# Optimization experiments

Measured on AMD Instinct MI355X. Metric: run time of the kernel, lower is better.

Reference implementation:

```python
import jax, jax.numpy as jnp
import numpy as np

H = 1024      # hidden_size
I = 2048      # intermediate_size
E = 8         # num_local_experts
TOP_K = 2     # num_experts_per_tok
B, S = 2, 2048


def setup_inputs() -> dict:
    key = jax.random.key(0)
    ks = jax.random.split(key, 9)
    sc = 0.02
    return {
        "hidden_states": jax.random.normal(ks[0], (B, S, H), dtype=jnp.float32),
        "router_w": jax.random.normal(ks[1], (H, E), dtype=jnp.float32) * sc,
        "gate_w": jax.random.normal(ks[2], (E, H, I), dtype=jnp.float32) * sc,
        "up_w": jax.random.normal(ks[3], (E, H, I), dtype=jnp.float32) * sc,
        "down_w": jax.random.normal(ks[4], (E, I, H), dtype=jnp.float32) * sc,
        "shared_gate_w": jax.random.normal(ks[5], (H, I), dtype=jnp.float32) * sc,
        "shared_up_w": jax.random.normal(ks[6], (H, I), dtype=jnp.float32) * sc,
        "shared_down_w": jax.random.normal(ks[7], (I, H), dtype=jnp.float32) * sc,
    }


def reference(hidden_states, router_w, gate_w, up_w, down_w,
              shared_gate_w, shared_up_w, shared_down_w):
    b, s, h = hidden_states.shape
    T = b * s
    x = hidden_states.reshape(T, h)

    # Router
    router_logits = x @ router_w                                   # [T, E]
    router_probs = jax.nn.softmax(router_logits.astype(jnp.float32), axis=-1).astype(x.dtype)
    topk_w, topk_i = jax.lax.top_k(router_probs, TOP_K)            # [T, K]
    topk_w = topk_w / jnp.sum(topk_w, axis=-1, keepdims=True)

    # Combine weights: combine[t, e] = sum of normalized top-k weight routed to expert e
    rows = jnp.arange(T)[:, None]
    combine = jnp.zeros((T, E), dtype=x.dtype).at[rows, topk_i].add(topk_w)  # [T, E]

    # Dense per-expert SwiGLU (combine weight is 0 for non-selected tokens, so
    # this matches the original gather-MLP-scatter math exactly)
    gate = jax.nn.silu(jnp.einsum('th,ehi->tei', x, gate_w))       # [T, E, I]
    up = jnp.einsum('th,ehi->tei', x, up_w)                        # [T, E, I]
    expert_out = jnp.einsum('tei,eih->teh', gate * up, down_w)     # [T, E, H]
    routed = jnp.einsum('te,teh->th', combine, expert_out)         # [T, H]

    # Shared expert (num_shared_experts = 1, mean over 1 is identity)
    shared = (jax.nn.silu(x @ shared_gate_w) * (x @ shared_up_w)) @ shared_down_w
    routed = routed + shared

    # Load-balance aux loss
    dispatch = jax.nn.one_hot(topk_i, E, dtype=jnp.float32).sum(axis=1) / float(TOP_K)  # [T, E]
    tokens_per_expert = dispatch.mean(axis=0)
    prob_per_expert = router_probs.astype(jnp.float32).mean(axis=0)
    aux_loss = E * jnp.sum(tokens_per_expert * prob_per_expert)

    # Router z-loss
    z_loss = jnp.mean(jax.nn.logsumexp(router_logits.astype(jnp.float32), axis=-1) ** 2)

    return (routed.reshape(b, s, h), aux_loss, z_loss,
            router_logits.reshape(b, s, E))
```

## Files before the change

kernel.cpp:

```cpp
#include <hip/hip_runtime.h>
#include <hip/hip_bf16.h>
#include <stdint.h>
#include <stddef.h>

typedef __bf16 bf16;
typedef __bf16 bf16x8 __attribute__((ext_vector_type(8)));
typedef __bf16 bf16x4 __attribute__((ext_vector_type(4)));
typedef float f32x4 __attribute__((ext_vector_type(4)));

#define HID 1024
#define IDIM 2048
#define NE 8
#define NTOK 4096
#define NSLOT 13312
#define SH_BASE 9216
#define MAX_TILES 104

#define WS_META    0
#define WS_PERM    4096
#define WS_TOKE    57344
#define WS_TOKW    90112
#define WS_SLOTOF  122880
#define WS_XBF     155648
#define WS_GATET   8544256
#define WS_UPT     42098688
#define WS_DOWNT   75653120
#define WS_SGT     109207552
#define WS_SUT     113401856
#define WS_SDT     117596160
#define WS_ACT     121790464
#define WS_DOUT    WS_GATET

#define M_CNT 0
#define M_CUR 8
#define M_PSUM 16
#define M_ZSUM 24
#define M_AOFF 32
#define M_NTILE 48
#define M_TE 64
#define M_TB 320

#define OUT_AUX 4194304
#define OUT_Z   4194305
#define OUT_LG  4194306

__device__ __forceinline__ int imin(int a, int b) { return a < b ? a : b; }

typedef const __attribute__((address_space(1))) uint32_t* as1_u32p;
typedef __attribute__((address_space(3))) uint32_t* as3_u32p;

__device__ __forceinline__ void gload16(const void* g, void* l) {
    __builtin_amdgcn_global_load_lds((as1_u32p)g, (as3_u32p)l, 16, 0, 0);
}

__global__ void zero_kernel(uint32_t* meta) {
    if (threadIdx.x < 32) meta[threadIdx.x] = 0;
}

__global__ __launch_bounds__(1024) void router_kernel(
    const float* __restrict__ x, const float* __restrict__ rw,
    float* __restrict__ out, uint32_t* meta, int* tok_e, float* tok_w,
    bf16* __restrict__ xbf)
{
    __shared__ float s_psum[NE];
    __shared__ float s_zsum;
    __shared__ uint32_t s_cnt[NE];
    int tid = threadIdx.x;
    if (tid < NE) { s_psum[tid] = 0.f; s_cnt[tid] = 0u; }
    if (tid == NE) s_zsum = 0.f;
    __syncthreads();

    int lane = tid & 63, wv = tid >> 6;
    int t = blockIdx.x * 16 + wv;
    float acc[NE];
#pragma unroll
    for (int e = 0; e < NE; e++) acc[e] = 0.f;
#pragma unroll
    for (int it = 0; it < 4; it++) {
        int h0 = (lane + it * 64) * 4;
        f32x4 xv = *(const f32x4*)&x[(size_t)t * HID + h0];
        bf16x4 xb;
#pragma unroll
        for (int j = 0; j < 4; j++) xb[j] = (bf16)xv[j];
        *(bf16x4*)&xbf[(size_t)t * HID + h0] = xb;
#pragma unroll
        for (int j = 0; j < 4; j++) {
            float xf = xv[j];
            const float* wrow = rw + (size_t)(h0 + j) * NE;
            f32x4 w0 = *(const f32x4*)wrow;
            f32x4 w1 = *(const f32x4*)(wrow + 4);
#pragma unroll
            for (int e = 0; e < 4; e++) { acc[e] += xf * w0[e]; acc[e + 4] += xf * w1[e]; }
        }
    }
#pragma unroll
    for (int off = 32; off >= 1; off >>= 1)
#pragma unroll
        for (int e = 0; e < NE; e++) acc[e] += __shfl_xor(acc[e], off);

    if (lane == 0) {
        float mx = acc[0];
        for (int e = 1; e < NE; e++) mx = fmaxf(mx, acc[e]);
        float p[NE], s = 0.f;
        for (int e = 0; e < NE; e++) { p[e] = __expf(acc[e] - mx); s += p[e]; }
        float lse = mx + __logf(s);
        atomicAdd(&s_zsum, lse * lse);
        float inv = 1.f / s;
        for (int e = 0; e < NE; e++) {
            p[e] *= inv;
            atomicAdd(&s_psum[e], p[e]);
            out[(size_t)OUT_LG + (size_t)t * NE + e] = acc[e];
        }
        int e0 = 0;
        for (int e = 1; e < NE; e++) if (p[e] > p[e0]) e0 = e;
        int e1 = (e0 == 0) ? 1 : 0;
        for (int e = 0; e < NE; e++) if (e != e0 && p[e] > p[e1]) e1 = e;
        float wn = 1.f / (p[e0] + p[e1]);
        tok_e[2 * t] = e0; tok_e[2 * t + 1] = e1;
        tok_w[2 * t] = p[e0] * wn; tok_w[2 * t + 1] = p[e1] * wn;
        atomicAdd(&s_cnt[e0], 1u);
        atomicAdd(&s_cnt[e1], 1u);
    }
    __syncthreads();
    if (tid < NE) {
        atomicAdd((float*)&meta[M_PSUM + tid], s_psum[tid]);
        atomicAdd(&meta[M_CNT + tid], s_cnt[tid]);
    }
    if (tid == NE) atomicAdd((float*)&meta[M_ZSUM], s_zsum);
}

__global__ void offsets_kernel(uint32_t* meta, float* out) {
    __shared__ uint32_t s_aoff[NE + 1];
    int lane = threadIdx.x;
    if (lane == 0) {
        uint32_t off = 0;
        for (int e = 0; e < NE; e++) {
            meta[M_AOFF + e] = off; s_aoff[e] = off;
            off += ((meta[M_CNT + e] + 127) >> 7) << 7;
        }
        meta[M_AOFF + NE] = off; s_aoff[NE] = off;
        float aux = 0.f;
        for (int e = 0; e < NE; e++) {
            float tpe = (float)meta[M_CNT + e] / (2.f * NTOK);
            float ppe = ((float*)meta)[M_PSUM + e] / (float)NTOK;
            aux += tpe * ppe;
        }
        out[OUT_AUX] = aux * NE;
        out[OUT_Z] = ((float*)meta)[M_ZSUM] / (float)NTOK;
    }
    __syncthreads();
    uint32_t nrt = s_aoff[NE] >> 7;
    uint32_t ntile = nrt + NTOK / 128;
    if (lane == 0) meta[M_NTILE] = ntile;
    for (uint32_t idx = lane; idx < ntile && idx < MAX_TILES; idx += 64) {
        if (idx < nrt) {
            uint32_t base = idx << 7, e = 0;
            for (int j = 1; j < NE; j++) if (base >= s_aoff[j]) e = j;
            meta[M_TE + idx] = e;
            meta[M_TB + idx] = base;
        } else {
            meta[M_TE + idx] = NE;
            meta[M_TB + idx] = SH_BASE + ((idx - nrt) << 7);
        }
    }
}

__global__ void fill_kernel(uint32_t* perm) {
    int g = blockIdx.x * 256 + threadIdx.x;
    if (g < NSLOT) perm[g] = (g < SH_BASE) ? 0u : (uint32_t)(g - SH_BASE);
}

__global__ void dispatch_kernel(uint32_t* meta, const int* tok_e,
                                uint32_t* perm, uint32_t* slot_of) {
    int t = blockIdx.x * 256 + threadIdx.x;
    int lane = threadIdx.x & 63;
    for (int k = 0; k < 2; k++) {
        int e = tok_e[2 * t + k] & 7;
#pragma unroll
        for (int ee = 0; ee < NE; ee++) {
            bool mine = (e == ee);
            unsigned long long mask = __ballot(mine);
            if (mask == 0ull) continue;
            int leader = __ffsll((unsigned long long)mask) - 1;
            uint32_t wbase = 0;
            if (lane == leader)
                wbase = atomicAdd(&meta[M_CUR + ee], (uint32_t)__popcll(mask));
            wbase = __shfl(wbase, leader);
            if (mine) {
                uint32_t myrank = (uint32_t)__popcll(mask & ((1ull << lane) - 1ull));
                uint32_t slot = meta[M_AOFF + ee] + wbase + myrank;
                if (slot >= NSLOT) slot = 0;
                perm[slot] = (uint32_t)t;
                slot_of[2 * t + k] = slot;
            }
        }
    }
}

__device__ __forceinline__ size_t f_off(int n, int k, int KB32) {
    return ((size_t)((n >> 5) * KB32 + (k >> 5)) * 2 + ((n >> 4) & 1)) * 512
         + (size_t)((((k >> 3) & 3) * 16 + (n & 15)) * 8);
}

__global__ __launch_bounds__(256) void transpose_kernel(
    const float* gw, const float* uw, const float* dw,
    const float* sg, const float* su, const float* sd, char* ws)
{
    int mat = blockIdx.x >> 9, tile = blockIdx.x & 511;
    const float* src; bf16* dst; int R, C;
    const size_t MSZ = (size_t)HID * IDIM;
    if (mat < 8)       { src = gw + mat * MSZ;        dst = (bf16*)(ws + WS_GATET) + mat * MSZ; R = HID;  C = IDIM; }
    else if (mat < 16) { src = uw + (mat - 8) * MSZ;  dst = (bf16*)(ws + WS_UPT) + (mat - 8) * MSZ; R = HID; C = IDIM; }
    else if (mat < 24) { src = dw + (mat - 16) * MSZ; dst = (bf16*)(ws + WS_DOWNT) + (mat - 16) * MSZ; R = IDIM; C = HID; }
    else if (mat == 24){ src = sg; dst = (bf16*)(ws + WS_SGT); R = HID; C = IDIM; }
    else if (mat == 25){ src = su; dst = (bf16*)(ws + WS_SUT); R = HID; C = IDIM; }
    else               { src = sd; dst = (bf16*)(ws + WS_SDT); R = IDIM; C = HID; }
    int KB32 = R >> 5;
    int tpr = C >> 6;
    int r0 = (tile / tpr) * 64, c0 = (tile % tpr) * 64;
    __shared__ bf16 tl[64][65];
    int tid = threadIdx.x;
#pragma unroll
    for (int it = 0; it < 4; it++) {
        int idx = tid + it * 256;
        int r = idx >> 4, c4 = (idx & 15) * 4;
        f32x4 v = *(const f32x4*)&src[(size_t)(r0 + r) * C + c0 + c4];
#pragma unroll
        for (int j = 0; j < 4; j++) tl[c4 + j][r] = (bf16)v[j];
    }
    __syncthreads();
#pragma unroll
    for (int it = 0; it < 2; it++) {
        int idx = tid + it * 256;
        int rr = idx >> 3, c8 = (idx & 7) * 8;
        int n = c0 + rr, k = r0 + c8;
        bf16x8 o;
#pragma unroll
        for (int j = 0; j < 8; j++) o[j] = tl[rr][c8 + j];
        *(bf16x8*)&dst[f_off(n, k, KB32)] = o;
    }
}

__global__ __launch_bounds__(256, 2) void stage1_kernel(char* __restrict__ ws)
{
    uint32_t* meta = (uint32_t*)(ws + WS_META);
    int mtile = blockIdx.y;
    int ntile = imin((int)meta[M_NTILE], MAX_TILES);
    if (mtile >= ntile) return;
    int e = imin((int)meta[M_TE + mtile], NE);
    int slot0 = imin((int)meta[M_TB + mtile], NSLOT - 128);
    if (slot0 < 0) slot0 = 0;
    const bf16* BgF = (e < NE) ? (const bf16*)(ws + WS_GATET) + (size_t)e * HID * IDIM
                               : (const bf16*)(ws + WS_SGT);
    const bf16* BuF = (e < NE) ? (const bf16*)(ws + WS_UPT) + (size_t)e * HID * IDIM
                               : (const bf16*)(ws + WS_SUT);
    const uint32_t* perm = (const uint32_t*)(ws + WS_PERM);
    const bf16* xbf = (const bf16*)(ws + WS_XBF);
    bf16* act = (bf16*)(ws + WS_ACT);

    __shared__ bf16 As[8192];
    __shared__ bf16 Bgs[8192];
    __shared__ bf16 Bus[8192];

    int tid = threadIdx.x, lane = tid & 63, wv = tid >> 6;
    int q = lane >> 4, m = lane & 15;

    int tok0 = (int)(perm[slot0 + wv * 16 + m] & (NTOK - 1));
    int tok1 = (int)(perm[slot0 + (wv + 4) * 16 + m] & (NTOK - 1));
    const bf16* gA0 = xbf + (size_t)tok0 * HID + q * 8;
    const bf16* gA1 = xbf + (size_t)tok1 * HID + q * 8;
    int N32 = blockIdx.x * 4 + wv;
    const bf16* gBg = BgF + (size_t)N32 * 32768 + lane * 8;
    const bf16* gBu = BuF + (size_t)N32 * 32768 + lane * 8;

    f32x4 zero4 = {0.f, 0.f, 0.f, 0.f};
    f32x4 accg[8][2], accu[8][2];
#pragma unroll
    for (int a = 0; a < 8; a++)
#pragma unroll
        for (int b = 0; b < 2; b++) { accg[a][b] = zero4; accu[a][b] = zero4; }

    for (int k0 = 0; k0 < HID; k0 += 64) {
        int kc = k0 >> 5;
        gload16(gA0 + k0,      &As[(wv * 2 + 0) * 512]);
        gload16(gA0 + k0 + 32, &As[(wv * 2 + 1) * 512]);
        gload16(gA1 + k0,      &As[((wv + 4) * 2 + 0) * 512]);
        gload16(gA1 + k0 + 32, &As[((wv + 4) * 2 + 1) * 512]);
#pragma unroll
        for (int nt = 0; nt < 2; nt++)
#pragma unroll
            for (int kk = 0; kk < 2; kk++) {
                size_t so = (size_t)(kc + kk) * 1024 + nt * 512;
                gload16(gBg + so, &Bgs[((wv * 2 + nt) * 2 + kk) * 512]);
                gload16(gBu + so, &Bus[((wv * 2 + nt) * 2 + kk) * 512]);
            }
        __syncthreads();
#pragma unroll
        for (int kk = 0; kk < 2; kk++) {
            bf16x8 af[8];
#pragma unroll
            for (int mc = 0; mc < 8; mc++)
                af[mc] = *(bf16x8*)&As[((mc * 2 + kk) * 64 + lane) * 8];
#pragma unroll
            for (int nt = 0; nt < 2; nt++) {
                bf16x8 bg = *(bf16x8*)&Bgs[(((wv * 2 + nt) * 2 + kk) * 64 + lane) * 8];
                bf16x8 bu = *(bf16x8*)&Bus[(((wv * 2 + nt) * 2 + kk) * 64 + lane) * 8];
#pragma unroll
                for (int mc = 0; mc < 8; mc++) {
                    accg[mc][nt] = __builtin_amdgcn_mfma_f32_16x16x32_bf16(af[mc], bg, accg[mc][nt], 0, 0, 0);
                    accu[mc][nt] = __builtin_amdgcn_mfma_f32_16x16x32_bf16(af[mc], bu, accu[mc][nt], 0, 0, 0);
                }
            }
        }
        __syncthreads();
    }
    int tile = slot0 >> 7;
    int kcell = blockIdx.x * 4 + wv;
    size_t tbase = (size_t)tile * 262144;
#pragma unroll
    for (int mc = 0; mc < 8; mc++)
#pragma unroll
        for (int nt = 0; nt < 2; nt++) {
            int kc2 = nt * 2 + (m >> 3);
            size_t base = tbase + (size_t)(kcell * 8 + mc) * 512
                        + (size_t)(kc2 * 16) * 8 + (m & 7);
#pragma unroll
            for (int r = 0; r < 4; r++) {
                float g = accg[mc][nt][r], u = accu[mc][nt][r];
                float v = g / (1.f + __expf(-g)) * u;
                act[base + (size_t)(q * 4 + r) * 8] = (bf16)v;
            }
        }
}

__global__ __launch_bounds__(256, 3) void stage2_kernel(char* __restrict__ ws)
{
    uint32_t* meta = (uint32_t*)(ws + WS_META);
    int mtile = blockIdx.y;
    int ntile = imin((int)meta[M_NTILE], MAX_TILES);
    if (mtile >= ntile) return;
    int e = imin((int)meta[M_TE + mtile], NE);
    int slot0 = imin((int)meta[M_TB + mtile], NSLOT - 128);
    if (slot0 < 0) slot0 = 0;
    int n0 = blockIdx.x * 128;
    const bf16* BF = (e < NE) ? (const bf16*)(ws + WS_DOWNT) + (size_t)e * HID * IDIM
                              : (const bf16*)(ws + WS_SDT);
    const bf16* actF = (const bf16*)(ws + WS_ACT);
    bf16* dout = (bf16*)(ws + WS_DOUT);

    __shared__ bf16 As[8192];
    __shared__ bf16 Bs[8192];

    int tid = threadIdx.x, lane = tid & 63, wv = tid >> 6;
    int q = lane >> 4, m = lane & 15;

    int tile = slot0 >> 7;
    size_t tbase = (size_t)tile * 262144;
    const bf16* gA = actF + tbase + lane * 8;
    int N32 = blockIdx.x * 4 + wv;
    const bf16* gB = BF + (size_t)N32 * 65536 + lane * 8;

    f32x4 zero4 = {0.f, 0.f, 0.f, 0.f};
    f32x4 acc[8][2];
#pragma unroll
    for (int a = 0; a < 8; a++)
#pragma unroll
        for (int b = 0; b < 2; b++) acc[a][b] = zero4;

    for (int k0 = 0; k0 < IDIM; k0 += 64) {
        int kc = k0 >> 5;
#pragma unroll
        for (int kk = 0; kk < 2; kk++) {
            gload16(gA + (size_t)((kc + kk) * 8 + wv) * 512,     &As[(wv * 2 + kk) * 512]);
            gload16(gA + (size_t)((kc + kk) * 8 + wv + 4) * 512, &As[((wv + 4) * 2 + kk) * 512]);
        }
#pragma unroll
        for (int nt = 0; nt < 2; nt++)
#pragma unroll
            for (int kk = 0; kk < 2; kk++)
                gload16(gB + (size_t)(kc + kk) * 1024 + nt * 512,
                        &Bs[((wv * 2 + nt) * 2 + kk) * 512]);
        __syncthreads();
#pragma unroll
        for (int kk = 0; kk < 2; kk++) {
            bf16x8 af[8];
#pragma unroll
            for (int mc = 0; mc < 8; mc++)
                af[mc] = *(bf16x8*)&As[((mc * 2 + kk) * 64 + lane) * 8];
#pragma unroll
            for (int nt = 0; nt < 2; nt++) {
                bf16x8 bfr = *(bf16x8*)&Bs[(((wv * 2 + nt) * 2 + kk) * 64 + lane) * 8];
#pragma unroll
                for (int mc = 0; mc < 8; mc++)
                    acc[mc][nt] = __builtin_amdgcn_mfma_f32_16x16x32_bf16(af[mc], bfr, acc[mc][nt], 0, 0, 0);
            }
        }
        __syncthreads();
    }
#pragma unroll
    for (int mc = 0; mc < 8; mc++)
#pragma unroll
        for (int nt = 0; nt < 2; nt++)
#pragma unroll
            for (int r = 0; r < 4; r++) {
                int slot = slot0 + mc * 16 + q * 4 + r;
                int col = n0 + wv * 32 + nt * 16 + m;
                dout[(size_t)slot * HID + col] = (bf16)acc[mc][nt][r];
            }
}

__global__ __launch_bounds__(256) void combine_kernel(char* __restrict__ ws, float* __restrict__ out)
{
    int g = blockIdx.x * 256 + threadIdx.x;
    int t = g >> 7;
    int hc = (g & 127) * 8;
    const uint32_t* slot_of = (const uint32_t*)(ws + WS_SLOTOF);
    const float* tok_w = (const float*)(ws + WS_TOKW);
    const bf16* dout = (const bf16*)(ws + WS_DOUT);
    uint32_t s0 = slot_of[2 * t], s1 = slot_of[2 * t + 1];
    if (s0 >= NSLOT) s0 = 0;
    if (s1 >= NSLOT) s1 = 0;
    float w0 = tok_w[2 * t], w1 = tok_w[2 * t + 1];
    bf16x8 a = *(const bf16x8*)&dout[(size_t)s0 * HID + hc];
    bf16x8 b = *(const bf16x8*)&dout[(size_t)s1 * HID + hc];
    bf16x8 c = *(const bf16x8*)&dout[(size_t)(SH_BASE + t) * HID + hc];
    f32x4 o0, o1;
#pragma unroll
    for (int j = 0; j < 4; j++)
        o0[j] = w0 * (float)a[j] + w1 * (float)b[j] + (float)c[j];
#pragma unroll
    for (int j = 0; j < 4; j++)
        o1[j] = w0 * (float)a[j + 4] + w1 * (float)b[j + 4] + (float)c[j + 4];
    *(f32x4*)&out[(size_t)t * HID + hc] = o0;
    *(f32x4*)&out[(size_t)t * HID + hc + 4] = o1;
}

extern "C" void kernel_launch(void* const* d_in, const int* in_sizes, int n_in,
                              void* d_out, int out_size, void* d_ws, size_t ws_size,
                              hipStream_t stream) {
    const float* x  = (const float*)d_in[0];
    const float* rw = (const float*)d_in[1];
    const float* gw = (const float*)d_in[2];
    const float* uw = (const float*)d_in[3];
    const float* dw = (const float*)d_in[4];
    const float* sg = (const float*)d_in[5];
    const float* su = (const float*)d_in[6];
    const float* sd = (const float*)d_in[7];
    float* out = (float*)d_out;
    char* ws = (char*)d_ws;
    uint32_t* meta = (uint32_t*)(ws + WS_META);
    uint32_t* perm = (uint32_t*)(ws + WS_PERM);
    int* tok_e = (int*)(ws + WS_TOKE);
    float* tok_w = (float*)(ws + WS_TOKW);
    uint32_t* slot_of = (uint32_t*)(ws + WS_SLOTOF);
    bf16* xbf = (bf16*)(ws + WS_XBF);

    hipLaunchKernelGGL(zero_kernel, dim3(1), dim3(64), 0, stream, meta);
    hipLaunchKernelGGL(router_kernel, dim3(NTOK / 16), dim3(1024), 0, stream,
                       x, rw, out, meta, tok_e, tok_w, xbf);
    hipLaunchKernelGGL(offsets_kernel, dim3(1), dim3(64), 0, stream, meta, out);
    hipLaunchKernelGGL(fill_kernel, dim3((NSLOT + 255) / 256), dim3(256), 0, stream, perm);
    hipLaunchKernelGGL(dispatch_kernel, dim3(NTOK / 256), dim3(256), 0, stream,
                       meta, tok_e, perm, slot_of);
    hipLaunchKernelGGL(transpose_kernel, dim3(27 * 512), dim3(256), 0, stream,
                       gw, uw, dw, sg, su, sd, ws);
    hipLaunchKernelGGL(stage1_kernel, dim3(IDIM / 128, MAX_TILES), dim3(256), 0, stream, ws);
    hipLaunchKernelGGL(stage2_kernel, dim3(HID / 128, MAX_TILES), dim3(256), 0, stream, ws);
    hipLaunchKernelGGL(combine_kernel, dim3(NTOK * HID / 8 / 256), dim3(256), 0, stream, ws, out);
}
```

Baseline: 509.1 us.

## Load MFMA operands directly from global memory, drop LDS staging in expert GEMMs

```diff
diff --git a/kernel.cpp b/kernel.cpp
--- a/kernel.cpp
+++ b/kernel.cpp
@@ -45,13 +45,6 @@
 #define OUT_LG  4194306
 
 __device__ __forceinline__ int imin(int a, int b) { return a < b ? a : b; }
-
-typedef const __attribute__((address_space(1))) uint32_t* as1_u32p;
-typedef __attribute__((address_space(3))) uint32_t* as3_u32p;
-
-__device__ __forceinline__ void gload16(const void* g, void* l) {
-    __builtin_amdgcn_global_load_lds((as1_u32p)g, (as3_u32p)l, 16, 0, 0);
-}
 
 __global__ void zero_kernel(uint32_t* meta) {
     if (threadIdx.x < 32) meta[threadIdx.x] = 0;
@@ -258,17 +251,15 @@
     const bf16* xbf = (const bf16*)(ws + WS_XBF);
     bf16* act = (bf16*)(ws + WS_ACT);
 
-    __shared__ bf16 As[8192];
-    __shared__ bf16 Bgs[8192];
-    __shared__ bf16 Bus[8192];
-
     int tid = threadIdx.x, lane = tid & 63, wv = tid >> 6;
     int q = lane >> 4, m = lane & 15;
 
-    int tok0 = (int)(perm[slot0 + wv * 16 + m] & (NTOK - 1));
-    int tok1 = (int)(perm[slot0 + (wv + 4) * 16 + m] & (NTOK - 1));
-    const bf16* gA0 = xbf + (size_t)tok0 * HID + q * 8;
-    const bf16* gA1 = xbf + (size_t)tok1 * HID + q * 8;
+    const bf16* ga[8];
+#pragma unroll
+    for (int mc = 0; mc < 8; mc++) {
+        int tok = (int)(perm[slot0 + mc * 16 + m] & (NTOK - 1));
+        ga[mc] = xbf + (size_t)tok * HID + q * 8;
+    }
     int N32 = blockIdx.x * 4 + wv;
     const bf16* gBg = BgF + (size_t)N32 * 32768 + lane * 8;
     const bf16* gBu = BuF + (size_t)N32 * 32768 + lane * 8;
@@ -280,39 +271,27 @@
 #pragma unroll
         for (int b = 0; b < 2; b++) { accg[a][b] = zero4; accu[a][b] = zero4; }
 
-    for (int k0 = 0; k0 < HID; k0 += 64) {
-        int kc = k0 >> 5;
-        gload16(gA0 + k0,      &As[(wv * 2 + 0) * 512]);
-        gload16(gA0 + k0 + 32, &As[(wv * 2 + 1) * 512]);
-        gload16(gA1 + k0,      &As[((wv + 4) * 2 + 0) * 512]);
-        gload16(gA1 + k0 + 32, &As[((wv + 4) * 2 + 1) * 512]);
-#pragma unroll
-        for (int nt = 0; nt < 2; nt++)
-#pragma unroll
-            for (int kk = 0; kk < 2; kk++) {
-                size_t so = (size_t)(kc + kk) * 1024 + nt * 512;
-                gload16(gBg + so, &Bgs[((wv * 2 + nt) * 2 + kk) * 512]);
-                gload16(gBu + so, &Bus[((wv * 2 + nt) * 2 + kk) * 512]);
+    for (int kc = 0; kc < 32; kc += 2) {
+#pragma unroll
+        for (int kk = 0; kk < 2; kk++) {
+            int k = (kc + kk) * 32;
+            bf16x8 af[8];
+#pragma unroll
+            for (int mc = 0; mc < 8; mc++)
+                af[mc] = *(const bf16x8*)(ga[mc] + k);
+            size_t bo = (size_t)(kc + kk) * 1024;
+            bf16x8 bg0 = *(const bf16x8*)(gBg + bo);
+            bf16x8 bg1 = *(const bf16x8*)(gBg + bo + 512);
+            bf16x8 bu0 = *(const bf16x8*)(gBu + bo);
+            bf16x8 bu1 = *(const bf16x8*)(gBu + bo + 512);
+#pragma unroll
+            for (int mc = 0; mc < 8; mc++) {
+                accg[mc][0] = __builtin_amdgcn_mfma_f32_16x16x32_bf16(af[mc], bg0, accg[mc][0], 0, 0, 0);
+                accg[mc][1] = __builtin_amdgcn_mfma_f32_16x16x32_bf16(af[mc], bg1, accg[mc][1], 0, 0, 0);
+                accu[mc][0] = __builtin_amdgcn_mfma_f32_16x16x32_bf16(af[mc], bu0, accu[mc][0], 0, 0, 0);
+                accu[mc][1] = __builtin_amdgcn_mfma_f32_16x16x32_bf16(af[mc], bu1, accu[mc][1], 0, 0, 0);
             }
-        __syncthreads();
-#pragma unroll
-        for (int kk = 0; kk < 2; kk++) {
-            bf16x8 af[8];
-#pragma unroll
-            for (int mc = 0; mc < 8; mc++)
-                af[mc] = *(bf16x8*)&As[((mc * 2 + kk) * 64 + lane) * 8];
-#pragma unroll
-            for (int nt = 0; nt < 2; nt++) {
-                bf16x8 bg = *(bf16x8*)&Bgs[(((wv * 2 + nt) * 2 + kk) * 64 + lane) * 8];
-                bf16x8 bu = *(bf16x8*)&Bus[(((wv * 2 + nt) * 2 + kk) * 64 + lane) * 8];
-#pragma unroll
-                for (int mc = 0; mc < 8; mc++) {
-                    accg[mc][nt] = __builtin_amdgcn_mfma_f32_16x16x32_bf16(af[mc], bg, accg[mc][nt], 0, 0, 0);
-                    accu[mc][nt] = __builtin_amdgcn_mfma_f32_16x16x32_bf16(af[mc], bu, accu[mc][nt], 0, 0, 0);
-                }
-            }
-        }
-        __syncthreads();
+        }
     }
     int tile = slot0 >> 7;
     int kcell = blockIdx.x * 4 + wv;
@@ -333,7 +312,7 @@
         }
 }
 
-__global__ __launch_bounds__(256, 3) void stage2_kernel(char* __restrict__ ws)
+__global__ __launch_bounds__(256, 2) void stage2_kernel(char* __restrict__ ws)
 {
     uint32_t* meta = (uint32_t*)(ws + WS_META);
     int mtile = blockIdx.y;
@@ -342,69 +321,58 @@
     int e = imin((int)meta[M_TE + mtile], NE);
     int slot0 = imin((int)meta[M_TB + mtile], NSLOT - 128);
     if (slot0 < 0) slot0 = 0;
-    int n0 = blockIdx.x * 128;
+    int n0 = blockIdx.x * 256;
     const bf16* BF = (e < NE) ? (const bf16*)(ws + WS_DOWNT) + (size_t)e * HID * IDIM
                               : (const bf16*)(ws + WS_SDT);
     const bf16* actF = (const bf16*)(ws + WS_ACT);
     bf16* dout = (bf16*)(ws + WS_DOUT);
 
-    __shared__ bf16 As[8192];
-    __shared__ bf16 Bs[8192];
-
     int tid = threadIdx.x, lane = tid & 63, wv = tid >> 6;
     int q = lane >> 4, m = lane & 15;
 
     int tile = slot0 >> 7;
-    size_t tbase = (size_t)tile * 262144;
-    const bf16* gA = actF + tbase + lane * 8;
-    int N32 = blockIdx.x * 4 + wv;
-    const bf16* gB = BF + (size_t)N32 * 65536 + lane * 8;
+    const bf16* gA = actF + (size_t)tile * 262144 + lane * 8;
+    int n32a = blockIdx.x * 8 + wv * 2;
+    const bf16* gB0 = BF + (size_t)n32a * 65536 + lane * 8;
+    const bf16* gB1 = BF + (size_t)(n32a + 1) * 65536 + lane * 8;
 
     f32x4 zero4 = {0.f, 0.f, 0.f, 0.f};
-    f32x4 acc[8][2];
+    f32x4 acc[8][4];
 #pragma unroll
     for (int a = 0; a < 8; a++)
 #pragma unroll
-        for (int b = 0; b < 2; b++) acc[a][b] = zero4;
-
-    for (int k0 = 0; k0 < IDIM; k0 += 64) {
-        int kc = k0 >> 5;
+        for (int b = 0; b < 4; b++) acc[a][b] = zero4;
+
+    for (int kc = 0; kc < 64; kc += 2) {
 #pragma unroll
         for (int kk = 0; kk < 2; kk++) {
-            gload16(gA + (size_t)((kc + kk) * 8 + wv) * 512,     &As[(wv * 2 + kk) * 512]);
-            gload16(gA + (size_t)((kc + kk) * 8 + wv + 4) * 512, &As[((wv + 4) * 2 + kk) * 512]);
-        }
-#pragma unroll
-        for (int nt = 0; nt < 2; nt++)
-#pragma unroll
-            for (int kk = 0; kk < 2; kk++)
-                gload16(gB + (size_t)(kc + kk) * 1024 + nt * 512,
-                        &Bs[((wv * 2 + nt) * 2 + kk) * 512]);
-        __syncthreads();
-#pragma unroll
-        for (int kk = 0; kk < 2; kk++) {
+            int kcc = kc + kk;
             bf16x8 af[8];
 #pragma unroll
             for (int mc = 0; mc < 8; mc++)
-                af[mc] = *(bf16x8*)&As[((mc * 2 + kk) * 64 + lane) * 8];
-#pragma unroll
-            for (int nt = 0; nt < 2; nt++) {
-                bf16x8 bfr = *(bf16x8*)&Bs[(((wv * 2 + nt) * 2 + kk) * 64 + lane) * 8];
-#pragma unroll
-                for (int mc = 0; mc < 8; mc++)
-                    acc[mc][nt] = __builtin_amdgcn_mfma_f32_16x16x32_bf16(af[mc], bfr, acc[mc][nt], 0, 0, 0);
+                af[mc] = *(const bf16x8*)(gA + (size_t)(kcc * 8 + mc) * 512);
+            size_t bo = (size_t)kcc * 1024;
+            bf16x8 b0 = *(const bf16x8*)(gB0 + bo);
+            bf16x8 b1 = *(const bf16x8*)(gB0 + bo + 512);
+            bf16x8 b2 = *(const bf16x8*)(gB1 + bo);
+            bf16x8 b3 = *(const bf16x8*)(gB1 + bo + 512);
+#pragma unroll
+            for (int mc = 0; mc < 8; mc++) {
+                acc[mc][0] = __builtin_amdgcn_mfma_f32_16x16x32_bf16(af[mc], b0, acc[mc][0], 0, 0, 0);
+                acc[mc][1] = __builtin_amdgcn_mfma_f32_16x16x32_bf16(af[mc], b1, acc[mc][1], 0, 0, 0);
+                acc[mc][2] = __builtin_amdgcn_mfma_f32_16x16x32_bf16(af[mc], b2, acc[mc][2], 0, 0, 0);
+                acc[mc][3] = __builtin_amdgcn_mfma_f32_16x16x32_bf16(af[mc], b3, acc[mc][3], 0, 0, 0);
             }
         }
-        __syncthreads();
     }
 #pragma unroll
     for (int mc = 0; mc < 8; mc++)
 #pragma unroll
-        for (int nt = 0; nt < 2; nt++)
+        for (int nt = 0; nt < 4; nt++)
 #pragma unroll
             for (int r = 0; r < 4; r++) {
                 int slot = slot0 + mc * 16 + q * 4 + r;
-                int col = n0 + wv * 32 + nt * 16 + m;
+                int col = n0 + wv * 64 + nt * 16 + m;
                 dout[(size_t)slot * HID + col] = (bf16)acc[mc][nt][r];
             }
 }
@@ -465,6 +433,6 @@
     hipLaunchKernelGGL(transpose_kernel, dim3(27 * 512), dim3(256), 0, stream,
                        gw, uw, dw, sg, su, sd, ws);
     hipLaunchKernelGGL(stage1_kernel, dim3(IDIM / 128, MAX_TILES), dim3(256), 0, stream, ws);
-    hipLaunchKernelGGL(stage2_kernel, dim3(HID / 128, MAX_TILES), dim3(256), 0, stream, ws);
+    hipLaunchKernelGGL(stage2_kernel, dim3(HID / 256, MAX_TILES), dim3(256), 0, stream, ws);
     hipLaunchKernelGGL(combine_kernel, dim3(NTOK * HID / 8 / 256), dim3(256), 0, stream, ws, out);
 }
```

After: 745.6 us. +46.5%, slower.
